# Performance work log

Measured on AMD Instinct MI355X. Metric: run time of the kernel, lower is better.

The kernel has to match this reference:

```python
import jax, jax.numpy as jnp
import numpy as np

IN_SIZE = 512
HID = 512
BATCH = 65536


def setup_inputs() -> dict:
    key = jax.random.key(0)
    ks = jax.random.split(key, 20)
    s = 1.0 / np.sqrt(IN_SIZE)
    sh = 1.0 / np.sqrt(HID)
    d = {
        "inputs": jax.random.normal(ks[0], (BATCH, IN_SIZE), jnp.float32),
        "state": jax.random.normal(ks[1], (BATCH, HID), jnp.float32),
        "parent_state": jax.random.normal(ks[2], (BATCH, HID), jnp.float32),
    }
    # input-path linears (with bias), torch Linear layout: W [out, in], y = x @ W.T + b
    for i, name in enumerate(["w_a", "w_r", "w_r1", "w_c"]):
        d[name + "_w"] = jax.random.uniform(ks[3 + 2 * i], (HID, IN_SIZE), jnp.float32, -s, s)
        d[name + "_b"] = jax.random.uniform(ks[4 + 2 * i], (HID,), jnp.float32, -s, s)
    # state-path and parent-path linears (no bias)
    for i, name in enumerate(["u_a", "u_r", "u_r1", "u_c", "p_a", "p_r", "p_r1", "p_c"]):
        d[name + "_w"] = jax.random.uniform(ks[11 + i], (HID, HID), jnp.float32, -sh, sh)
    return d


def reference(inputs, state, parent_state,
              w_a_w, w_a_b, w_r_w, w_r_b, w_r1_w, w_r1_b, w_c_w, w_c_b,
              u_a_w, u_r_w, u_r1_w, u_c_w,
              p_a_w, p_r_w, p_r1_w, p_c_w):
    def lin(x, w, b=None):
        y = x @ w.T
        return y if b is None else y + b

    att = jax.nn.sigmoid(lin(inputs, w_a_w, w_a_b) + lin(state, u_a_w) + lin(parent_state, p_a_w))
    r = jax.nn.sigmoid(lin(inputs, w_r_w, w_r_b) + lin(state, u_r_w) + lin(parent_state, p_r_w))
    r1 = jax.nn.sigmoid(lin(inputs, w_r1_w, w_r1_b) + lin(state, u_r1_w) + lin(parent_state, p_r1_w))
    c = jnp.tanh(lin(inputs, w_c_w, w_c_b) + lin(state * r, u_c_w) + lin(parent_state * r1, p_c_w))
    new_h = att * c + (1.0 - att) * state
    return new_h
```

## Files before the change

### kernel.cpp

```cpp
#include <hip/hip_runtime.h>
#include <stdint.h>


typedef unsigned short u16;
using bf16x8 = __attribute__((ext_vector_type(8))) __bf16;
using f32x4  = __attribute__((ext_vector_type(4))) float;

__device__ __forceinline__ u16 f2bf(float f) {
    __bf16 b = (__bf16)f;
    union { __bf16 b; u16 u; } v; v.b = b;
    return v.u;
}
__device__ __forceinline__ uint32_t f2bf2(float lo, float hi) {
    return (uint32_t)f2bf(lo) | ((uint32_t)f2bf(hi) << 16);
}
__device__ __forceinline__ float bf2f(u16 s) {
    union { uint32_t u; float f; } v; v.u = ((uint32_t)s) << 16;
    return v.f;
}
__device__ __forceinline__ void load_lds16(const void* g, void* l) {
    __builtin_amdgcn_global_load_lds(
        (const __attribute__((address_space(1))) uint32_t*)g,
        (__attribute__((address_space(3))) uint32_t*)l, 16, 0, 0);
}

__global__ void prep_weights(
    const float* __restrict__ wa, const float* __restrict__ ua, const float* __restrict__ pa,
    const float* __restrict__ wrg, const float* __restrict__ ur, const float* __restrict__ pr,
    const float* __restrict__ wr1, const float* __restrict__ ur1, const float* __restrict__ pr1,
    const float* __restrict__ wcc, const float* __restrict__ uc, const float* __restrict__ pc,
    u16* __restrict__ B1, u16* __restrict__ B2)
{
    int idx = blockIdx.x * 256 + threadIdx.x;
    const int T1 = 1536 * 1536;
    if (idx < T1) {
        int n = idx / 1536, k = idx - n * 1536;
        int g = n >> 9, nn = n & 511;
        int o = k >> 9, kk = k & 511;
        const float* s;
        if (g == 0)      s = (o == 0) ? wa  : (o == 1) ? ua  : pa;
        else if (g == 1) s = (o == 0) ? wrg : (o == 1) ? ur  : pr;
        else             s = (o == 0) ? wr1 : (o == 1) ? ur1 : pr1;
        B1[idx] = f2bf(s[nn * 512 + kk]);
    } else {
        int j = idx - T1;
        if (j < 512 * 1536) {
            int n = j / 1536, k = j - n * 1536;
            int o = k >> 9, kk = k & 511;
            const float* s = (o == 0) ? wcc : (o == 1) ? uc : pc;
            B2[j] = f2bf(s[n * 512 + kk]);
        }
    }
}

__global__ void cast_inputs(const float* __restrict__ X, const float* __restrict__ H,
                            const float* __restrict__ P,
                            u16* __restrict__ Xb, u16* __restrict__ Hb, u16* __restrict__ Pb)
{
    const long long MAT8 = (65536LL * 512) / 8;
    for (long long t = (long long)blockIdx.x * 256 + threadIdx.x;
         t < 3 * MAT8; t += (long long)gridDim.x * 256) {
        int m = (int)(t >> 22);
        long long e = (t & (MAT8 - 1)) * 8;
        const float* s = (m == 0) ? X : (m == 1) ? H : P;
        u16* d = (m == 0) ? Xb : (m == 1) ? Hb : Pb;
        f32x4 a = *(const f32x4*)(s + e);
        f32x4 b = *(const f32x4*)(s + e + 4);
        uint4 q;
        q.x = f2bf2(a.x, a.y); q.y = f2bf2(a.z, a.w);
        q.z = f2bf2(b.x, b.y); q.w = f2bf2(b.z, b.w);
        *(uint4*)(d + e) = q;
    }
}

template<int MODE>
__global__ __launch_bounds__(256, 4)
void g128(const u16* __restrict__ A0, const u16* __restrict__ A1s, const u16* __restrict__ A2s,
          const u16* __restrict__ Bw,
          const float* __restrict__ bias0, const float* __restrict__ bias1,
          const float* __restrict__ bias2,
          const u16* __restrict__ HbP, const u16* __restrict__ PbP,
          u16* __restrict__ attb, u16* __restrict__ hrw, u16* __restrict__ pr1w,
          float* __restrict__ outp)
{
    __shared__ u16 Ab[128 * 64];
    __shared__ u16 Bb[128 * 64];

    const int tid  = threadIdx.x;
    const int lane = tid & 63;
    const int w    = tid >> 6;
    const int wr   = w >> 1;
    const int wc   = w & 1;

    int panel, ntl;
    const int xcd = blockIdx.x & 7;
    const int idx = blockIdx.x >> 3;
    if (MODE == 1) {
        const int mg = xcd >> 1, ng = xcd & 1;
        panel = mg * 128 + idx / 6;
        ntl   = ng * 6 + idx % 6;
    } else {
        panel = xcd * 64 + (idx >> 2);
        ntl   = idx & 3;
    }
    const int m0 = panel * 128;
    const int n0 = ntl * 128;

    const int srow = w * 32 + (lane >> 3);
    const int scol = ((lane & 7) ^ (lane >> 3)) * 8;
    const int ofsA = srow * 512  + scol;
    const int ofsB = srow * 1536 + scol;
    const u16* const bA0 = A0  + (size_t)m0 * 512;
    const u16* const bA1 = A1s + (size_t)m0 * 512;
    const u16* const bA2 = A2s + (size_t)m0 * 512;
    const u16* const bB  = Bw  + (size_t)n0 * 1536;

    auto issueA = [&](int kt) {
        const u16* src = (kt < 8) ? bA0 : (kt < 16) ? bA1 : bA2;
        const u16* g = src + (kt & 7) * 64 + ofsA;
        u16* lb = &Ab[(w * 32) * 64];
#pragma unroll
        for (int c = 0; c < 4; ++c)
            load_lds16(g + c * 8 * 512, lb + c * 8 * 64);
    };
    auto issueB = [&](int kt) {
        const u16* g = bB + kt * 64 + ofsB;
        u16* lb = &Bb[(w * 32) * 64];
#pragma unroll
        for (int c = 0; c < 4; ++c)
            load_lds16(g + c * 8 * 1536, lb + c * 8 * 64);
    };

    f32x4 acc[4][4];
    const f32x4 vz = {0.0f, 0.0f, 0.0f, 0.0f};
#pragma unroll
    for (int i = 0; i < 4; ++i)
#pragma unroll
        for (int j = 0; j < 4; ++j) acc[i][j] = vz;

    auto compute = [&]() {
        const int rsw = (lane & 7) << 3;
        const int rb  = lane & 15;
        const int hi8 = (lane >> 4) * 8;
#pragma unroll
        for (int ks = 0; ks < 2; ++ks) {
            bf16x8 af[4], bfr[4];
            const int col = (ks * 32 + hi8) ^ rsw;
#pragma unroll
            for (int fm = 0; fm < 4; ++fm)
                af[fm] = *(const bf16x8*)&Ab[(wr * 64 + fm * 16 + rb) * 64 + col];
#pragma unroll
            for (int fn = 0; fn < 4; ++fn)
                bfr[fn] = *(const bf16x8*)&Bb[(wc * 64 + fn * 16 + rb) * 64 + col];
#pragma unroll
            for (int fm = 0; fm < 4; ++fm)
#pragma unroll
                for (int fn = 0; fn < 4; ++fn)
                    acc[fm][fn] = __builtin_amdgcn_mfma_f32_16x16x32_bf16(
                        af[fm], bfr[fn], acc[fm][fn], 0, 0, 0);
        }
    };

#pragma unroll 1
    for (int kt = 0; kt < 24; ++kt) {
        issueA(kt); issueB(kt);
        __syncthreads();
        compute();
        __syncthreads();
    }

    const int rl = (lane >> 4) * 4;
    const int cl = lane & 15;
    const int rb0 = m0 + wr * 64 + rl;
    if (MODE == 1) {
        const int gate = ntl >> 2;
        const float* bias = (gate == 0) ? bias0 : (gate == 1) ? bias1 : bias2;
        const int nnb = (ntl & 3) * 128 + wc * 64;
#pragma unroll
        for (int fm = 0; fm < 4; ++fm)
#pragma unroll
            for (int fn = 0; fn < 4; ++fn) {
                const int nn = nnb + fn * 16 + cl;
                const float b = bias[nn];
                int off = (rb0 + fm * 16) * 512 + nn;
#pragma unroll
                for (int j = 0; j < 4; ++j, off += 512) {
                    float v = acc[fm][fn][j] + b;
                    float s = 1.0f / (1.0f + __expf(-v));
                    if (gate == 0)      attb[off] = f2bf(s);
                    else if (gate == 1) hrw[off]  = f2bf(s * bf2f(HbP[off]));
                    else                pr1w[off] = f2bf(s * bf2f(PbP[off]));
                }
            }
    } else {
        const int nnb = n0 + wc * 64;
#pragma unroll
        for (int fm = 0; fm < 4; ++fm)
#pragma unroll
            for (int fn = 0; fn < 4; ++fn) {
                const int nn = nnb + fn * 16 + cl;
                const float b = bias0[nn];
                int off = (rb0 + fm * 16) * 512 + nn;
#pragma unroll
                for (int j = 0; j < 4; ++j, off += 512) {
                    float v = acc[fm][fn][j] + b;
                    float e = __expf(2.0f * v);
                    float ct = 1.0f - 2.0f / (e + 1.0f);
                    float a = bf2f(attb[off]);
                    float h = bf2f(HbP[off]);
                    outp[off] = a * ct + (1.0f - a) * h;
                }
            }
    }
}

__global__ __launch_bounds__(256, 2)
void k1_small(const float* __restrict__ X, const float* __restrict__ H,
              const float* __restrict__ P, const u16* __restrict__ B1,
              const float* __restrict__ ba, const float* __restrict__ br,
              const float* __restrict__ br1,
              float* __restrict__ attf, u16* __restrict__ hrw, u16* __restrict__ pr1w)
{
    __shared__ u16 Ab[2][128 * 64];
    __shared__ u16 Bb[2][128 * 64];
    const int tid = threadIdx.x, lane = tid & 63, w = tid >> 6;
    const int wr = w >> 1, wc = w & 1;
    const int bid = blockIdx.x, xcd = bid & 7, idx = bid >> 3;
    const int panel = idx / 12, ntl = idx - panel * 12;
    const int m0 = (xcd * 64 + panel) * 128, n0 = ntl * 128;
    const int srow = w * 32 + (lane >> 3);
    const int scol = ((lane & 7) ^ (lane >> 3)) * 8;
    const int arow = tid >> 4, acol = (tid & 15) * 4;
    const int aswz = acol ^ ((arow & 7) << 3);
    f32x4 acc[4][4];
    const f32x4 vz = {0, 0, 0, 0};
#pragma unroll
    for (int i = 0; i < 4; ++i)
#pragma unroll
        for (int j = 0; j < 4; ++j) acc[i][j] = vz;
    f32x4 areg[8];
    auto issueA = [&](int kt) {
        const float* src = (kt < 8) ? X : (kt < 16) ? H : P;
        const float* base = src + (size_t)(m0 + arow) * 512 + (kt & 7) * 64 + acol;
#pragma unroll
        for (int rr = 0; rr < 8; ++rr)
            areg[rr] = *(const f32x4*)(base + (size_t)(rr * 16) * 512);
    };
    auto writeA = [&](int nb) {
#pragma unroll
        for (int rr = 0; rr < 8; ++rr) {
            uint2 q; q.x = f2bf2(areg[rr].x, areg[rr].y);
            q.y = f2bf2(areg[rr].z, areg[rr].w);
            *(uint2*)&Ab[nb][(arow + rr * 16) * 64 + aswz] = q;
        }
    };
    auto issueB = [&](int kt, int nb) {
        const u16* gb = B1 + (size_t)(n0 + srow) * 1536 + kt * 64 + scol;
        u16* lb = &Bb[nb][(w * 32) * 64];
#pragma unroll
        for (int c = 0; c < 4; ++c)
            load_lds16(gb + (size_t)c * 8 * 1536, lb + c * 8 * 64);
    };
    auto compute = [&](int cb) {
        const int rsw = (lane & 7) << 3, rb = lane & 15, hi8 = (lane >> 4) * 8;
#pragma unroll
        for (int ks = 0; ks < 2; ++ks) {
            bf16x8 af[4], bfr[4];
            const int col = (ks * 32 + hi8) ^ rsw;
#pragma unroll
            for (int fm = 0; fm < 4; ++fm)
                af[fm] = *(const bf16x8*)&Ab[cb][(wr * 64 + fm * 16 + rb) * 64 + col];
#pragma unroll
            for (int fn = 0; fn < 4; ++fn)
                bfr[fn] = *(const bf16x8*)&Bb[cb][(wc * 64 + fn * 16 + rb) * 64 + col];
#pragma unroll
            for (int fm = 0; fm < 4; ++fm)
#pragma unroll
                for (int fn = 0; fn < 4; ++fn)
                    acc[fm][fn] = __builtin_amdgcn_mfma_f32_16x16x32_bf16(
                        af[fm], bfr[fn], acc[fm][fn], 0, 0, 0);
        }
    };
    issueA(0); issueB(0, 0); writeA(0);
    __syncthreads();
    int cb = 0;
#pragma unroll 2
    for (int kt = 0; kt < 24; ++kt) {
        if (kt < 23) { issueA(kt + 1); issueB(kt + 1, cb ^ 1); }
        compute(cb);
        if (kt < 23) writeA(cb ^ 1);
        __syncthreads();
        cb ^= 1;
    }
    const int gate = ntl >> 2;
    const float* bias = (gate == 0) ? ba : (gate == 1) ? br : br1;
    const int nnb = (ntl & 3) * 128 + wc * 64;
    const int rl = (lane >> 4) * 4, cl = lane & 15;
#pragma unroll
    for (int fm = 0; fm < 4; ++fm)
#pragma unroll
        for (int fn = 0; fn < 4; ++fn) {
            const int nn = nnb + fn * 16 + cl;
            const float b = bias[nn];
#pragma unroll
            for (int j = 0; j < 4; ++j) {
                const int row = m0 + wr * 64 + fm * 16 + rl + j;
                const size_t off = (size_t)row * 512 + nn;
                float v = acc[fm][fn][j] + b;
                float s = 1.0f / (1.0f + __expf(-v));
                if (gate == 0)      attf[off] = s;
                else if (gate == 1) hrw[off]  = f2bf(s * H[off]);
                else                pr1w[off] = f2bf(s * P[off]);
            }
        }
}

__global__ __launch_bounds__(256, 2)
void k2_small(const float* __restrict__ X, const float* __restrict__ H,
              const u16* __restrict__ B2, const float* __restrict__ bc,
              const u16* __restrict__ hrw, const u16* __restrict__ pr1w,
              float* outp)
{
    __shared__ u16 Ab[2][128 * 64];
    __shared__ u16 Bb[2][128 * 64];
    const int tid = threadIdx.x, lane = tid & 63, w = tid >> 6;
    const int wr = w >> 1, wc = w & 1;
    const int bid = blockIdx.x, xcd = bid & 7, idx = bid >> 3;
    const int panel = idx >> 2, ntl = idx & 3;
    const int m0 = (xcd * 64 + panel) * 128, n0 = ntl * 128;
    const int srow = w * 32 + (lane >> 3);
    const int scol = ((lane & 7) ^ (lane >> 3)) * 8;
    const int arow = tid >> 4, acol = (tid & 15) * 4;
    const int aswz = acol ^ ((arow & 7) << 3);
    f32x4 acc[4][4];
    const f32x4 vz = {0, 0, 0, 0};
#pragma unroll
    for (int i = 0; i < 4; ++i)
#pragma unroll
        for (int j = 0; j < 4; ++j) acc[i][j] = vz;
    f32x4 areg[8];
    auto issueA = [&](int kt, int nb) {
        if (kt >= 8) {
            const u16* src = (kt < 16) ? hrw : pr1w;
            const u16* gb = src + (size_t)(m0 + srow) * 512 + (kt & 7) * 64 + scol;
            u16* lb = &Ab[nb][(w * 32) * 64];
#pragma unroll
            for (int c = 0; c < 4; ++c)
                load_lds16(gb + (size_t)c * 8 * 512, lb + c * 8 * 64);
        } else {
            const float* base = X + (size_t)(m0 + arow) * 512 + (kt & 7) * 64 + acol;
#pragma unroll
            for (int rr = 0; rr < 8; ++rr)
                areg[rr] = *(const f32x4*)(base + (size_t)(rr * 16) * 512);
        }
    };
    auto writeA = [&](int kt, int nb) {
        if (kt < 8) {
#pragma unroll
            for (int rr = 0; rr < 8; ++rr) {
                uint2 q; q.x = f2bf2(areg[rr].x, areg[rr].y);
                q.y = f2bf2(areg[rr].z, areg[rr].w);
                *(uint2*)&Ab[nb][(arow + rr * 16) * 64 + aswz] = q;
            }
        }
    };
    auto issueB = [&](int kt, int nb) {
        const u16* gb = B2 + (size_t)(n0 + srow) * 1536 + kt * 64 + scol;
        u16* lb = &Bb[nb][(w * 32) * 64];
#pragma unroll
        for (int c = 0; c < 4; ++c)
            load_lds16(gb + (size_t)c * 8 * 1536, lb + c * 8 * 64);
    };
    auto compute = [&](int cb) {
        const int rsw = (lane & 7) << 3, rb = lane & 15, hi8 = (lane >> 4) * 8;
#pragma unroll
        for (int ks = 0; ks < 2; ++ks) {
            bf16x8 af[4], bfr[4];
            const int col = (ks * 32 + hi8) ^ rsw;
#pragma unroll
            for (int fm = 0; fm < 4; ++fm)
                af[fm] = *(const bf16x8*)&Ab[cb][(wr * 64 + fm * 16 + rb) * 64 + col];
#pragma unroll
            for (int fn = 0; fn < 4; ++fn)
                bfr[fn] = *(const bf16x8*)&Bb[cb][(wc * 64 + fn * 16 + rb) * 64 + col];
#pragma unroll
            for (int fm = 0; fm < 4; ++fm)
#pragma unroll
                for (int fn = 0; fn < 4; ++fn)
                    acc[fm][fn] = __builtin_amdgcn_mfma_f32_16x16x32_bf16(
                        af[fm], bfr[fn], acc[fm][fn], 0, 0, 0);
        }
    };
    issueA(0, 0); issueB(0, 0); writeA(0, 0);
    __syncthreads();
    int cb = 0;
#pragma unroll 2
    for (int kt = 0; kt < 24; ++kt) {
        if (kt < 23) { issueA(kt + 1, cb ^ 1); issueB(kt + 1, cb ^ 1); }
        compute(cb);
        if (kt < 23) writeA(kt + 1, cb ^ 1);
        __syncthreads();
        cb ^= 1;
    }
    const int nnb = n0 + wc * 64;
    const int rl = (lane >> 4) * 4, cl = lane & 15;
#pragma unroll
    for (int fm = 0; fm < 4; ++fm)
#pragma unroll
        for (int fn = 0; fn < 4; ++fn) {
            const int nn = nnb + fn * 16 + cl;
            const float b = bc[nn];
#pragma unroll
            for (int j = 0; j < 4; ++j) {
                const int row = m0 + wr * 64 + fm * 16 + rl + j;
                const size_t off = (size_t)row * 512 + nn;
                float v = acc[fm][fn][j] + b;
                float e = __expf(2.0f * v);
                float ct = 1.0f - 2.0f / (e + 1.0f);
                float a = outp[off];
                outp[off] = a * ct + (1.0f - a) * H[off];
            }
        }
}

extern "C" void kernel_launch(void* const* d_in, const int* in_sizes, int n_in,
                              void* d_out, int out_size, void* d_ws, size_t ws_size,
                              hipStream_t stream)
{
    const float* X   = (const float*)d_in[0];
    const float* H   = (const float*)d_in[1];
    const float* P   = (const float*)d_in[2];
    const float* wa  = (const float*)d_in[3];
    const float* ba  = (const float*)d_in[4];
    const float* wrg = (const float*)d_in[5];
    const float* br  = (const float*)d_in[6];
    const float* wr1 = (const float*)d_in[7];
    const float* br1 = (const float*)d_in[8];
    const float* wcc = (const float*)d_in[9];
    const float* bc  = (const float*)d_in[10];
    const float* ua  = (const float*)d_in[11];
    const float* ur  = (const float*)d_in[12];
    const float* ur1 = (const float*)d_in[13];
    const float* uc  = (const float*)d_in[14];
    const float* pa  = (const float*)d_in[15];
    const float* pr  = (const float*)d_in[16];
    const float* pr1 = (const float*)d_in[17];
    const float* pc  = (const float*)d_in[18];

    char* ws = (char*)d_ws;
    u16* B1   = (u16*)(ws);
    u16* B2   = (u16*)(ws + (size_t)4718592);
    u16* hrp  = (u16*)(ws + (size_t)6291456);
    u16* pr1p = (u16*)(ws + (size_t)73400320);
    u16* Xb   = (u16*)(ws + (size_t)140509184);
    u16* Hb   = (u16*)(ws + (size_t)207618048);
    u16* Pb   = (u16*)(ws + (size_t)274726912);
    u16* attb = (u16*)(ws + (size_t)341835776);
    float* out = (float*)d_out;

    const bool big3 = ws_size >= (size_t)408944640ULL;

    prep_weights<<<12288, 256, 0, stream>>>(wa, ua, pa, wrg, ur, pr, wr1, ur1, pr1,
                                            wcc, uc, pc, B1, B2);
    if (big3) {
        cast_inputs<<<3072, 256, 0, stream>>>(X, H, P, Xb, Hb, Pb);
        g128<1><<<6144, 256, 0, stream>>>(Xb, Hb, Pb, B1, ba, br, br1,
                                          Hb, Pb, attb, hrp, pr1p, out);
        g128<2><<<2048, 256, 0, stream>>>(Xb, hrp, pr1p, B2, bc, nullptr, nullptr,
                                          Hb, nullptr, attb, nullptr, nullptr, out);
    } else {
        k1_small<<<6144, 256, 0, stream>>>(X, H, P, B1, ba, br, br1, out, hrp, pr1p);
        k2_small<<<2048, 256, 0, stream>>>(X, H, B2, bc, hrp, pr1p, out);
    }
}
```

Before: 688.8 us.

## Double-buffer A tile in LDS and prefetch next k-step with partial waitcnt

Adds a second LDS buffer for the A operand and issues the global-to-LDS load for the next k-tile before computing the current one. An explicit s_waitcnt vmcnt(4) waits only for the current tile's loads, and plain s_barrier replaces __syncthreads. The goal is to overlap A-tile memory latency with MFMA work. The extra LDS forces launch bounds down from 4 to 3 blocks per CU, which lowers occupancy. The B tile is still loaded synchronously each iteration.

Measured after the change: 716.9 us. 1.04x slower.

```diff
diff --git a/kernel.cpp b/kernel.cpp
--- a/kernel.cpp
+++ b/kernel.cpp
@@ -22,6 +22,11 @@
     __builtin_amdgcn_global_load_lds(
         (const __attribute__((address_space(1))) uint32_t*)g,
         (__attribute__((address_space(3))) uint32_t*)l, 16, 0, 0);
+}
+__device__ __forceinline__ void fence_bar() {
+    asm volatile("" ::: "memory");
+    __builtin_amdgcn_s_barrier();
+    asm volatile("" ::: "memory");
 }
 
 __global__ void prep_weights(
@@ -74,7 +79,7 @@
 }
 
 template<int MODE>
-__global__ __launch_bounds__(256, 4)
+__global__ __launch_bounds__(256, 3)
 void g128(const u16* __restrict__ A0, const u16* __restrict__ A1s, const u16* __restrict__ A2s,
           const u16* __restrict__ Bw,
           const float* __restrict__ bias0, const float* __restrict__ bias1,
@@ -83,7 +88,7 @@
           u16* __restrict__ attb, u16* __restrict__ hrw, u16* __restrict__ pr1w,
           float* __restrict__ outp)
 {
-    __shared__ u16 Ab[128 * 64];
+    __shared__ u16 Ap[2][128 * 64];
     __shared__ u16 Bb[128 * 64];
 
     const int tid  = threadIdx.x;
@@ -115,10 +120,10 @@
     const u16* const bA2 = A2s + (size_t)m0 * 512;
     const u16* const bB  = Bw  + (size_t)n0 * 1536;
 
-    auto issueA = [&](int kt) {
+    auto issueA = [&](int kt, int p) {
         const u16* src = (kt < 8) ? bA0 : (kt < 16) ? bA1 : bA2;
         const u16* g = src + (kt & 7) * 64 + ofsA;
-        u16* lb = &Ab[(w * 32) * 64];
+        u16* lb = &Ap[p][(w * 32) * 64];
 #pragma unroll
         for (int c = 0; c < 4; ++c)
             load_lds16(g + c * 8 * 512, lb + c * 8 * 64);
@@ -138,7 +143,7 @@
 #pragma unroll
         for (int j = 0; j < 4; ++j) acc[i][j] = vz;
 
-    auto compute = [&]() {
+    auto compute = [&](int p) {
         const int rsw = (lane & 7) << 3;
         const int rb  = lane & 15;
         const int hi8 = (lane >> 4) * 8;
@@ -148,7 +153,7 @@
             const int col = (ks * 32 + hi8) ^ rsw;
 #pragma unroll
             for (int fm = 0; fm < 4; ++fm)
-                af[fm] = *(const bf16x8*)&Ab[(wr * 64 + fm * 16 + rb) * 64 + col];
+                af[fm] = *(const bf16x8*)&Ap[p][(wr * 64 + fm * 16 + rb) * 64 + col];
 #pragma unroll
             for (int fn = 0; fn < 4; ++fn)
                 bfr[fn] = *(const bf16x8*)&Bb[(wc * 64 + fn * 16 + rb) * 64 + col];
@@ -161,12 +166,21 @@
         }
     };
 
+    issueA(0, 0);
+    int pp = 0;
 #pragma unroll 1
     for (int kt = 0; kt < 24; ++kt) {
-        issueA(kt); issueB(kt);
-        __syncthreads();
-        compute();
-        __syncthreads();
+        issueB(kt);
+        if (kt < 23) {
+            issueA(kt + 1, pp ^ 1);
+            asm volatile("s_waitcnt vmcnt(4)" ::: "memory");
+        } else {
+            asm volatile("s_waitcnt vmcnt(0)" ::: "memory");
+        }
+        fence_bar();
+        compute(pp);
+        fence_bar();
+        pp ^= 1;
     }
 
     const int rl = (lane >> 4) * 4;
```
